# Kernel optimization log

Hardware: AMD Instinct MI355X
Metric: run time of the kernel (lower is better)

Reference implementation:

```python
import jax, jax.numpy as jnp
import numpy as np

N_NODES = 50000
N_EDGES = 512000
D = 128          # node_state_dim
H = 256          # edge hidden / message dim = 2*D (GRU input size)


def _edge_mlp(x, W1, b1, W2, b2):
    # Linear -> ReLU -> Linear, matching nn.Sequential built in build_model
    h = jax.nn.relu(x @ W1.T + b1)
    return h @ W2.T + b2


def _prop_once(node_states, f_idx, t_idx, W1, b1, W2, b2):
    # gather endpoints, concat, edge MLP, scatter-add into destination nodes
    edge_in = jnp.concatenate([node_states[f_idx], node_states[t_idx]], axis=-1)  # [E, 2D]
    msgs = _edge_mlp(edge_in, W1, b1, W2, b2)                                     # [E, H]
    return jax.ops.segment_sum(msgs, t_idx, num_segments=N_NODES)                 # [N, H]


def _gru_cell(x, h, W_ih, W_hh, b_ih, b_hh):
    # PyTorch GRU cell convention
    gi = x @ W_ih.T + b_ih   # [N, 3D]
    gh = h @ W_hh.T + b_hh   # [N, 3D]
    ir, iz, inn = jnp.split(gi, 3, axis=-1)
    hr, hz, hn = jnp.split(gh, 3, axis=-1)
    r = jax.nn.sigmoid(ir + hr)
    z = jax.nn.sigmoid(iz + hz)
    n = jnp.tanh(inn + r * hn)
    return (1.0 - z) * n + z * h


def setup_inputs() -> dict:
    key = jax.random.key(0)
    ks = jax.random.split(key, 16)
    s = 0.1  # edge_net_init_scale-ish small init
    inp = {
        "node_states": jax.random.normal(ks[0], (N_NODES, D), dtype=jnp.float32),
        "from_idx": jax.random.randint(ks[1], (N_EDGES,), 0, N_NODES),
        "to_idx": jax.random.randint(ks[2], (N_EDGES,), 0, N_NODES),
        # forward message net: Linear(2D->H), Linear(H->H)
        "Wf1": jax.random.normal(ks[3], (H, 2 * D), dtype=jnp.float32) * s,
        "bf1": jnp.zeros((H,), jnp.float32),
        "Wf2": jax.random.normal(ks[4], (H, H), dtype=jnp.float32) * s,
        "bf2": jnp.zeros((H,), jnp.float32),
        # reverse message net (separate params)
        "Wr1": jax.random.normal(ks[5], (H, 2 * D), dtype=jnp.float32) * s,
        "br1": jnp.zeros((H,), jnp.float32),
        "Wr2": jax.random.normal(ks[6], (H, H), dtype=jnp.float32) * s,
        "br2": jnp.zeros((H,), jnp.float32),
        # GRU(input=2D, hidden=D) params, torch layout
        "W_ih": jax.random.normal(ks[7], (3 * D, 2 * D), dtype=jnp.float32) * 0.05,
        "W_hh": jax.random.normal(ks[8], (3 * D, D), dtype=jnp.float32) * 0.05,
        "b_ih": jnp.zeros((3 * D,), jnp.float32),
        "b_hh": jnp.zeros((3 * D,), jnp.float32),
    }
    return inp


def reference(node_states, from_idx, to_idx, Wf1, bf1, Wf2, bf2,
              Wr1, br1, Wr2, br2, W_ih, W_hh, b_ih, b_hh):
    agg = _prop_once(node_states, from_idx, to_idx, Wf1, bf1, Wf2, bf2)
    agg = agg + _prop_once(node_states, to_idx, from_idx, Wr1, br1, Wr2, br2)
    return _gru_cell(agg, node_states, W_ih, W_hh, b_ih, b_hh)  # [N, D]
```

## Files before the change

### kernel.cpp

```cpp
#include <hip/hip_runtime.h>
#include <stdint.h>


#define NN 50000
#define NE 512000
#define SCAN_N (2 * NN)
#define SCAN_BLOCKS ((SCAN_N + 1023) / 1024)

typedef unsigned short u16;
typedef unsigned int u32;
using h8  = __attribute__((ext_vector_type(8))) _Float16;
using f4v = __attribute__((ext_vector_type(4))) float;

__device__ __forceinline__ float h2f(u16 u) {
  _Float16 h; __builtin_memcpy(&h, &u, 2); return (float)h;
}
__device__ __forceinline__ u16 f2h(float f) {
  _Float16 h = (_Float16)f; u16 u; __builtin_memcpy(&u, &h, 2); return u;
}
__device__ __forceinline__ float4 load4h(const u16* p) {
  ushort4 u = *(const ushort4*)p;
  return make_float4(h2f(u.x), h2f(u.y), h2f(u.z), h2f(u.w));
}


__global__ void k_wcat(const float* __restrict__ Wf1, const float* __restrict__ bf1,
                       const float* __restrict__ Wr1, const float* __restrict__ br1,
                       u16* __restrict__ Wc16, float* __restrict__ biascat) {
  int c = blockIdx.x;
  int k = threadIdx.x;
  const float* src;
  if (c < 256)      src = Wf1 + (size_t)c * 256;
  else if (c < 512) src = Wr1 + (size_t)(c - 256) * 256 + 128;
  else if (c < 768) src = Wf1 + (size_t)(c - 512) * 256 + 128;
  else              src = Wr1 + (size_t)(c - 768) * 256;
  float v = src[k];
  int nt = c >> 4, kt = k >> 5, g = (k & 31) >> 3, j = k & 7;
  int lane = (c & 15) + g * 16;
  Wc16[((size_t)nt * 4 + kt) * 512 + lane * 8 + j] = f2h(v);
  if (k == 0) biascat[c] = (c < 256) ? bf1[c] : ((c >= 768) ? br1[c - 768] : 0.f);
}

__global__ void k_gcat(const float* __restrict__ W_ih, const float* __restrict__ Wf2,
                       const float* __restrict__ Wr2, u16* __restrict__ G16) {
  int b = blockIdx.x;
  int c = b % 384, w = b / 384;
  const float* W2 = w ? Wr2 : Wf2;
  int k = threadIdx.x;
  float acc = 0.f;
  for (int o = 0; o < 256; ++o)
    acc = fmaf(W_ih[(size_t)c * 256 + o], W2[(size_t)o * 256 + k], acc);
  int kg = w * 256 + k;
  int nt = c >> 4, kt = kg >> 5, g = (kg & 31) >> 3, j = kg & 7;
  int lane = (c & 15) + g * 16;
  G16[((size_t)nt * 16 + kt) * 512 + lane * 8 + j] = f2h(acc);
}

__global__ void k_whh(const float* __restrict__ W_hh, u16* __restrict__ Wh16) {
  int c = blockIdx.x, k = threadIdx.x;
  float v = W_hh[(size_t)c * 128 + k];
  int nt = c >> 4, kt = k >> 5, g = (k & 31) >> 3, j = k & 7;
  int lane = (c & 15) + g * 16;
  Wh16[((size_t)nt * 4 + kt) * 512 + lane * 8 + j] = f2h(v);
}

__global__ void k_vbias(const float* __restrict__ W_ih, const float* __restrict__ bf2,
                        const float* __restrict__ br2, float* __restrict__ vf,
                        float* __restrict__ vr) {
  int c = blockIdx.x * blockDim.x + threadIdx.x;
  if (c >= 384) return;
  float a = 0.f, b = 0.f;
  for (int o = 0; o < 256; ++o) {
    float w = W_ih[(size_t)c * 256 + o];
    a = fmaf(w, bf2[o], a);
    b = fmaf(w, br2[o], b);
  }
  vf[c] = a; vr[c] = b;
}

__global__ void k_nsh(const float* __restrict__ ns, u16* __restrict__ nsf) {
  int t = blockIdx.x * 256 + threadIdx.x;
  int n = t >> 4, kk8 = t & 15;
  float4 v0 = *(const float4*)(ns + (size_t)n * 128 + kk8 * 8);
  float4 v1 = *(const float4*)(ns + (size_t)n * 128 + kk8 * 8 + 4);
  u16 hv[8] = {f2h(v0.x), f2h(v0.y), f2h(v0.z), f2h(v0.w),
               f2h(v1.x), f2h(v1.y), f2h(v1.z), f2h(v1.w)};
  int mt = n >> 4, r = n & 15, kt = kk8 >> 2, g = kk8 & 3;
  int lane = r + g * 16;
  *(uint4*)(nsf + ((size_t)mt * 4 + kt) * 512 + lane * 8) = *(const uint4*)hv;
}

__global__ void k_hist(const int* __restrict__ from, const int* __restrict__ to,
                       int* __restrict__ cnt) {
  int e = blockIdx.x * 256 + threadIdx.x;
  if (e < NE) {
    atomicAdd(cnt + to[e], 1);
    atomicAdd(cnt + NN + from[e], 1);
  }
}

__global__ __launch_bounds__(256) void k_scanA(const int* __restrict__ cnt,
                                               int* __restrict__ bsum) {
  __shared__ int part[256];
  int b = blockIdx.x, tid = threadIdx.x;
  int idx = b * 1024 + tid * 4;
  int s = 0;
  if (idx + 3 < SCAN_N) {
    int4 v = *(const int4*)(cnt + idx);
    s = v.x + v.y + v.z + v.w;
  } else {
    for (int q = 0; q < 4; ++q)
      if (idx + q < SCAN_N) s += cnt[idx + q];
  }
  part[tid] = s;
  __syncthreads();
  for (int d = 128; d > 0; d >>= 1) {
    if (tid < d) part[tid] += part[tid + d];
    __syncthreads();
  }
  if (tid == 0) bsum[b] = part[0];
}

__global__ __launch_bounds__(128) void k_scanB(int* __restrict__ bsum) {
  __shared__ int part[128];
  int tid = threadIdx.x;
  int v = (tid < SCAN_BLOCKS) ? bsum[tid] : 0;
  part[tid] = v;
  __syncthreads();
  for (int d = 1; d < 128; d <<= 1) {
    int x = (tid >= d) ? part[tid - d] : 0;
    __syncthreads();
    part[tid] += x;
    __syncthreads();
  }
  if (tid < SCAN_BLOCKS) bsum[tid] = (tid > 0) ? part[tid - 1] : 0;
}

__global__ __launch_bounds__(256) void k_scanC(const int* __restrict__ cnt,
                                               const int* __restrict__ bsum,
                                               int* __restrict__ off,
                                               int* __restrict__ cur) {
  __shared__ int part[256];
  int b = blockIdx.x, tid = threadIdx.x;
  int idx = b * 1024 + tid * 4;
  int c[4] = {0, 0, 0, 0};
  if (idx + 3 < SCAN_N) {
    int4 v = *(const int4*)(cnt + idx);
    c[0] = v.x; c[1] = v.y; c[2] = v.z; c[3] = v.w;
  } else {
    for (int q = 0; q < 4; ++q)
      if (idx + q < SCAN_N) c[q] = cnt[idx + q];
  }
  int s = c[0] + c[1] + c[2] + c[3];
  part[tid] = s;
  __syncthreads();
  for (int d = 1; d < 256; d <<= 1) {
    int x = (tid >= d) ? part[tid - d] : 0;
    __syncthreads();
    part[tid] += x;
    __syncthreads();
  }
  int run = bsum[b] + ((tid > 0) ? part[tid - 1] : 0);
#pragma unroll
  for (int q = 0; q < 4; ++q) {
    if (idx + q < SCAN_N) {
      off[idx + q] = run;
      cur[idx + q] = run;
      run += c[q];
    }
  }
  if (b == 0 && tid == 0) off[SCAN_N] = 2 * NE;
}

__global__ void k_fill(const int* __restrict__ from, const int* __restrict__ to,
                       int* __restrict__ cur, int* __restrict__ nbr) {
  int e = blockIdx.x * 256 + threadIdx.x;
  if (e < NE) {
    int f = from[e], t = to[e];
    nbr[atomicAdd(cur + t, 1)] = f;
    nbr[atomicAdd(cur + NN + f, 1)] = t;
  }
}

__global__ __launch_bounds__(256) void k_proj(const u16* __restrict__ nsf,
                                              const u16* __restrict__ Wc16,
                                              const float* __restrict__ biascat,
                                              u16* __restrict__ T) {
  const int w = threadIdx.x >> 6, lane = threadIdx.x & 63;
  const int mt0 = blockIdx.x * 4;
  const int nt0 = blockIdx.y * 16 + w * 4;
  const h8 hzv = {(_Float16)0.f, (_Float16)0.f, (_Float16)0.f, (_Float16)0.f,
                  (_Float16)0.f, (_Float16)0.f, (_Float16)0.f, (_Float16)0.f};
  f4v acc[4][4];
#pragma unroll
  for (int m = 0; m < 4; ++m)
#pragma unroll
    for (int n = 0; n < 4; ++n) acc[m][n] = (f4v){0.f, 0.f, 0.f, 0.f};

#pragma unroll
  for (int kt = 0; kt < 4; ++kt) {
    h8 a[4], b[4];
#pragma unroll
    for (int m = 0; m < 4; ++m) {
      int mt = mt0 + m;
      a[m] = (mt < 3125) ? *(const h8*)(nsf + ((size_t)mt * 4 + kt) * 512 + lane * 8) : hzv;
    }
#pragma unroll
    for (int n = 0; n < 4; ++n)
      b[n] = *(const h8*)(Wc16 + ((size_t)(nt0 + n) * 4 + kt) * 512 + lane * 8);
#pragma unroll
    for (int m = 0; m < 4; ++m)
#pragma unroll
      for (int n = 0; n < 4; ++n)
        acc[m][n] = __builtin_amdgcn_mfma_f32_16x16x32_f16(a[m], b[n], acc[m][n], 0, 0, 0);
  }

  const int c0 = lane & 15, rB = (lane >> 4) * 4;
#pragma unroll
  for (int m = 0; m < 4; ++m) {
    int mt = mt0 + m;
    if (mt >= 3125) continue;
#pragma unroll
    for (int n = 0; n < 4; ++n) {
      int col = (nt0 + n) * 16 + c0;
      float bias = biascat[col];
#pragma unroll
      for (int reg = 0; reg < 4; ++reg) {
        int row = mt * 16 + rB + reg;
        T[(size_t)row * 1024 + col] = f2h(acc[m][n][reg] + bias);
      }
    }
  }
}

__global__ __launch_bounds__(256) void k_gather(const u16* __restrict__ T,
                                                const int* __restrict__ nbr,
                                                const int* __restrict__ off,
                                                u16* __restrict__ Sf) {
  const int lane = threadIdx.x & 63;
  const int gid = blockIdx.x * 4 + (threadIdx.x >> 6);
  const int n = gid >> 1, dir = gid & 1;
  const u16* Tn = T + (size_t)n * 1024;
  const int mt = n >> 4, r = n & 15;
  const int g = (lane & 7) >> 1, j0 = (lane & 1) * 4;
  const int laneF = r + g * 16;

  const int invofs = dir ? 256 : 512;
  const int gofs = dir ? 768 : 0;
  float4 inv = load4h(Tn + invofs + lane * 4);
  const int s = off[dir * NN + n];
  const int e = off[dir * NN + n + 1];
  float4 a0 = make_float4(0.f, 0.f, 0.f, 0.f);
  float4 a1 = make_float4(0.f, 0.f, 0.f, 0.f);
  float4 a2 = make_float4(0.f, 0.f, 0.f, 0.f);
  float4 a3 = make_float4(0.f, 0.f, 0.f, 0.f);
  for (int i = s; i < e; i += 64) {
    int nb = (i + lane < e) ? nbr[i + lane] : 0;
    int cnt = min(64, e - i);
    int k = 0;
    for (; k + 3 < cnt; k += 4) {
      int f0 = __shfl(nb, k);
      int f1 = __shfl(nb, k + 1);
      int f2 = __shfl(nb, k + 2);
      int f3 = __shfl(nb, k + 3);
      float4 v0 = load4h(T + (size_t)f0 * 1024 + gofs + lane * 4);
      float4 v1 = load4h(T + (size_t)f1 * 1024 + gofs + lane * 4);
      float4 v2 = load4h(T + (size_t)f2 * 1024 + gofs + lane * 4);
      float4 v3 = load4h(T + (size_t)f3 * 1024 + gofs + lane * 4);
      a0.x += fmaxf(inv.x + v0.x, 0.f); a1.x += fmaxf(inv.x + v1.x, 0.f);
      a0.y += fmaxf(inv.y + v0.y, 0.f); a1.y += fmaxf(inv.y + v1.y, 0.f);
      a0.z += fmaxf(inv.z + v0.z, 0.f); a1.z += fmaxf(inv.z + v1.z, 0.f);
      a0.w += fmaxf(inv.w + v0.w, 0.f); a1.w += fmaxf(inv.w + v1.w, 0.f);
      a2.x += fmaxf(inv.x + v2.x, 0.f); a3.x += fmaxf(inv.x + v3.x, 0.f);
      a2.y += fmaxf(inv.y + v2.y, 0.f); a3.y += fmaxf(inv.y + v3.y, 0.f);
      a2.z += fmaxf(inv.z + v2.z, 0.f); a3.z += fmaxf(inv.z + v3.z, 0.f);
      a2.w += fmaxf(inv.w + v2.w, 0.f); a3.w += fmaxf(inv.w + v3.w, 0.f);
    }
    for (; k < cnt; ++k) {
      int f0 = __shfl(nb, k);
      float4 v0 = load4h(T + (size_t)f0 * 1024 + gofs + lane * 4);
      a0.x += fmaxf(inv.x + v0.x, 0.f);
      a0.y += fmaxf(inv.y + v0.y, 0.f);
      a0.z += fmaxf(inv.z + v0.z, 0.f);
      a0.w += fmaxf(inv.w + v0.w, 0.f);
    }
  }
  a0.x += a1.x + a2.x + a3.x;
  a0.y += a1.y + a2.y + a3.y;
  a0.z += a1.z + a2.z + a3.z;
  a0.w += a1.w + a2.w + a3.w;
  int kt = dir * 8 + (lane >> 3);
  u16 hv[4] = {f2h(a0.x), f2h(a0.y), f2h(a0.z), f2h(a0.w)};
  *(ushort4*)(Sf + ((size_t)mt * 16 + kt) * 512 + laneF * 8 + j0) = *(const ushort4*)hv;
}

__global__ __launch_bounds__(256) void k_gru(const u16* __restrict__ Sf,
                                             const u16* __restrict__ nsf,
                                             const u16* __restrict__ G16,
                                             const u16* __restrict__ Wh16,
                                             const float* __restrict__ ns,
                                             const float* __restrict__ b_ih,
                                             const float* __restrict__ b_hh,
                                             const float* __restrict__ vf,
                                             const float* __restrict__ vr,
                                             const int* __restrict__ off,
                                             float* __restrict__ out) {
  const int w = threadIdx.x >> 6, lane = threadIdx.x & 63;
  const int mt = blockIdx.x >> 1, half = blockIdx.x & 1;
  const int base = half * 4 + w;

  f4v gh[3], gi[3];
#pragma unroll
  for (int g = 0; g < 3; ++g) {
    gh[g] = (f4v){0.f, 0.f, 0.f, 0.f};
    gi[g] = (f4v){0.f, 0.f, 0.f, 0.f};
  }

#pragma unroll
  for (int kt = 0; kt < 4; ++kt) {
    h8 a = *(const h8*)(nsf + ((size_t)mt * 4 + kt) * 512 + lane * 8);
#pragma unroll
    for (int g = 0; g < 3; ++g) {
      h8 b = *(const h8*)(Wh16 + ((size_t)(base + 8 * g) * 4 + kt) * 512 + lane * 8);
      gh[g] = __builtin_amdgcn_mfma_f32_16x16x32_f16(a, b, gh[g], 0, 0, 0);
    }
  }

#pragma unroll
  for (int kt = 0; kt < 16; ++kt) {
    h8 a = *(const h8*)(Sf + ((size_t)mt * 16 + kt) * 512 + lane * 8);
#pragma unroll
    for (int g = 0; g < 3; ++g) {
      h8 b = *(const h8*)(G16 + ((size_t)(base + 8 * g) * 16 + kt) * 512 + lane * 8);
      gi[g] = __builtin_amdgcn_mfma_f32_16x16x32_f16(a, b, gi[g], 0, 0, 0);
    }
  }

  const int c0 = lane & 15, rB = (lane >> 4) * 4;
  const int d = base * 16 + c0;
  const float vf0 = vf[d], vf1 = vf[128 + d], vf2 = vf[256 + d];
  const float vr0 = vr[d], vr1 = vr[128 + d], vr2 = vr[256 + d];
  const float bi0 = b_ih[d], bi1 = b_ih[128 + d], bi2 = b_ih[256 + d];
  const float bh0 = b_hh[d], bh1 = b_hh[128 + d], bh2 = b_hh[256 + d];
#pragma unroll
  for (int reg = 0; reg < 4; ++reg) {
    int row = mt * 16 + rB + reg;
    float idg = (float)(off[row + 1] - off[row]);
    float odg = (float)(off[NN + row + 1] - off[NN + row]);
    float gr = gi[0][reg] + idg * vf0 + odg * vr0 + bi0;
    float gz = gi[1][reg] + idg * vf1 + odg * vr1 + bi1;
    float gn = gi[2][reg] + idg * vf2 + odg * vr2 + bi2;
    float hr = gh[0][reg] + bh0;
    float hzv = gh[1][reg] + bh1;
    float hn = gh[2][reg] + bh2;
    float rg = 1.f / (1.f + __expf(-(gr + hr)));
    float zg = 1.f / (1.f + __expf(-(gz + hzv)));
    float ng = tanhf(gn + rg * hn);
    float h = ns[(size_t)row * 128 + d];
    out[(size_t)row * 128 + d] = (1.f - zg) * ng + zg * h;
  }
}

extern "C" void kernel_launch(void* const* d_in, const int* in_sizes, int n_in,
                              void* d_out, int out_size, void* d_ws, size_t ws_size,
                              hipStream_t stream) {
  const float* ns   = (const float*)d_in[0];
  const int* from   = (const int*)d_in[1];
  const int* to     = (const int*)d_in[2];
  const float* Wf1  = (const float*)d_in[3];
  const float* bf1  = (const float*)d_in[4];
  const float* Wf2  = (const float*)d_in[5];
  const float* bf2  = (const float*)d_in[6];
  const float* Wr1  = (const float*)d_in[7];
  const float* br1  = (const float*)d_in[8];
  const float* Wr2  = (const float*)d_in[9];
  const float* br2  = (const float*)d_in[10];
  const float* W_ih = (const float*)d_in[11];
  const float* W_hh = (const float*)d_in[12];
  const float* b_ih = (const float*)d_in[13];
  const float* b_hh = (const float*)d_in[14];
  float* out = (float*)d_out;

  char* w = (char*)d_ws;
  u16*   Wc16    = (u16*)(w + 0);
  float* biascat = (float*)(w + 262144);
  u16*   G16     = (u16*)(w + 266240);
  u16*   Wh16    = (u16*)(w + 659456);
  float* vf      = (float*)(w + 757760);
  float* vr      = (float*)(w + 759296);
  int*   cnt     = (int*)(w + 760832);
  int*   off     = (int*)(w + 1160960);
  int*   cur     = (int*)(w + 1561088);
  int*   bsum    = (int*)(w + 1961216);
  int*   nbr     = (int*)(w + 1961728);
  u16*   nsf     = (u16*)(w + 6057728);
  u16*   T       = (u16*)(w + 18857728);
  u16*   Sf      = (u16*)(w + 121257728);

  hipMemsetAsync(cnt, 0, 400000, stream);

  k_wcat<<<1024, 128, 0, stream>>>(Wf1, bf1, Wr1, br1, Wc16, biascat);
  k_gcat<<<768, 256, 0, stream>>>(W_ih, Wf2, Wr2, G16);
  k_whh<<<384, 128, 0, stream>>>(W_hh, Wh16);
  k_vbias<<<3, 128, 0, stream>>>(W_ih, bf2, br2, vf, vr);
  k_nsh<<<3125, 256, 0, stream>>>(ns, nsf);

  k_hist<<<(NE + 255) / 256, 256, 0, stream>>>(from, to, cnt);
  k_scanA<<<SCAN_BLOCKS, 256, 0, stream>>>(cnt, bsum);
  k_scanB<<<1, 128, 0, stream>>>(bsum);
  k_scanC<<<SCAN_BLOCKS, 256, 0, stream>>>(cnt, bsum, off, cur);
  k_fill<<<(NE + 255) / 256, 256, 0, stream>>>(from, to, cur, nbr);

  k_proj<<<dim3(782, 4), 256, 0, stream>>>(nsf, Wc16, biascat, T);
  k_gather<<<25000, 256, 0, stream>>>(T, nbr, off, Sf);
  k_gru<<<6250, 256, 0, stream>>>(Sf, nsf, G16, Wh16, ns, b_ih, b_hh, vf, vr, off, out);
}
```

Before: 363.9 us.

## Use packed fp16 add/relu in gather and two row tiles per GRU wave

The gather kernel now keeps neighbor rows in fp16 and applies add+ReLU with packed half2 ops. It also unrolls to 8 outstanding loads per iteration to raise memory-level parallelism. The GRU kernel processes two 16-row tiles per wave, so each weight fragment load feeds two MFMAs, and the grid is halved. This trades more registers per wave and fp16 rounding of the pre-activation sum for fewer weight loads and fewer conversions.

```diff
diff --git a/kernel.cpp b/kernel.cpp
--- a/kernel.cpp
+++ b/kernel.cpp
@@ -9,6 +9,8 @@
 
 typedef unsigned short u16;
 typedef unsigned int u32;
+using h2  = __attribute__((ext_vector_type(2))) _Float16;
+using h4  = __attribute__((ext_vector_type(4))) _Float16;
 using h8  = __attribute__((ext_vector_type(8))) _Float16;
 using f4v = __attribute__((ext_vector_type(4))) float;
 
@@ -17,10 +19,6 @@
 }
 __device__ __forceinline__ u16 f2h(float f) {
   _Float16 h = (_Float16)f; u16 u; __builtin_memcpy(&u, &h, 2); return u;
-}
-__device__ __forceinline__ float4 load4h(const u16* p) {
-  ushort4 u = *(const ushort4*)p;
-  return make_float4(h2f(u.x), h2f(u.y), h2f(u.z), h2f(u.w));
 }
 
 
@@ -247,50 +245,66 @@
 
   const int invofs = dir ? 256 : 512;
   const int gofs = dir ? 768 : 0;
-  float4 inv = load4h(Tn + invofs + lane * 4);
+  const h2 z2 = {(_Float16)0.f, (_Float16)0.f};
+  h4 invv = *(const h4*)(Tn + invofs + lane * 4);
+  h2 inv01 = {invv[0], invv[1]};
+  h2 inv23 = {invv[2], invv[3]};
   const int s = off[dir * NN + n];
   const int e = off[dir * NN + n + 1];
-  float4 a0 = make_float4(0.f, 0.f, 0.f, 0.f);
-  float4 a1 = make_float4(0.f, 0.f, 0.f, 0.f);
-  float4 a2 = make_float4(0.f, 0.f, 0.f, 0.f);
-  float4 a3 = make_float4(0.f, 0.f, 0.f, 0.f);
+  float a0 = 0.f, a1 = 0.f, a2 = 0.f, a3 = 0.f;
+
   for (int i = s; i < e; i += 64) {
     int nb = (i + lane < e) ? nbr[i + lane] : 0;
     int cnt = min(64, e - i);
     int k = 0;
-    for (; k + 3 < cnt; k += 4) {
-      int f0 = __shfl(nb, k);
-      int f1 = __shfl(nb, k + 1);
-      int f2 = __shfl(nb, k + 2);
-      int f3 = __shfl(nb, k + 3);
-      float4 v0 = load4h(T + (size_t)f0 * 1024 + gofs + lane * 4);
-      float4 v1 = load4h(T + (size_t)f1 * 1024 + gofs + lane * 4);
-      float4 v2 = load4h(T + (size_t)f2 * 1024 + gofs + lane * 4);
-      float4 v3 = load4h(T + (size_t)f3 * 1024 + gofs + lane * 4);
-      a0.x += fmaxf(inv.x + v0.x, 0.f); a1.x += fmaxf(inv.x + v1.x, 0.f);
-      a0.y += fmaxf(inv.y + v0.y, 0.f); a1.y += fmaxf(inv.y + v1.y, 0.f);
-      a0.z += fmaxf(inv.z + v0.z, 0.f); a1.z += fmaxf(inv.z + v1.z, 0.f);
-      a0.w += fmaxf(inv.w + v0.w, 0.f); a1.w += fmaxf(inv.w + v1.w, 0.f);
-      a2.x += fmaxf(inv.x + v2.x, 0.f); a3.x += fmaxf(inv.x + v3.x, 0.f);
-      a2.y += fmaxf(inv.y + v2.y, 0.f); a3.y += fmaxf(inv.y + v3.y, 0.f);
-      a2.z += fmaxf(inv.z + v2.z, 0.f); a3.z += fmaxf(inv.z + v3.z, 0.f);
-      a2.w += fmaxf(inv.w + v2.w, 0.f); a3.w += fmaxf(inv.w + v3.w, 0.f);
+    for (; k + 7 < cnt; k += 8) {
+      h4 wv[8];
+#pragma unroll
+      for (int q = 0; q < 8; ++q) {
+        int f = __shfl(nb, k + q);
+        wv[q] = *(const h4*)(T + (size_t)f * 1024 + gofs + lane * 4);
+      }
+#pragma unroll
+      for (int q = 0; q < 8; ++q) {
+        h2 t01 = {wv[q][0], wv[q][1]};
+        h2 t23 = {wv[q][2], wv[q][3]};
+        t01 = __builtin_elementwise_max(t01 + inv01, z2);
+        t23 = __builtin_elementwise_max(t23 + inv23, z2);
+        a0 += (float)t01[0]; a1 += (float)t01[1];
+        a2 += (float)t23[0]; a3 += (float)t23[1];
+      }
+    }
+    if (k + 3 < cnt) {
+      h4 wv[4];
+#pragma unroll
+      for (int q = 0; q < 4; ++q) {
+        int f = __shfl(nb, k + q);
+        wv[q] = *(const h4*)(T + (size_t)f * 1024 + gofs + lane * 4);
+      }
+#pragma unroll
+      for (int q = 0; q < 4; ++q) {
+        h2 t01 = {wv[q][0], wv[q][1]};
+        h2 t23 = {wv[q][2], wv[q][3]};
+        t01 = __builtin_elementwise_max(t01 + inv01, z2);
+        t23 = __builtin_elementwise_max(t23 + inv23, z2);
+        a0 += (float)t01[0]; a1 += (float)t01[1];
+        a2 += (float)t23[0]; a3 += (float)t23[1];
+      }
+      k += 4;
     }
     for (; k < cnt; ++k) {
-      int f0 = __shfl(nb, k);
-      float4 v0 = load4h(T + (size_t)f0 * 1024 + gofs + lane * 4);
-      a0.x += fmaxf(inv.x + v0.x, 0.f);
-      a0.y += fmaxf(inv.y + v0.y, 0.f);
-      a0.z += fmaxf(inv.z + v0.z, 0.f);
-      a0.w += fmaxf(inv.w + v0.w, 0.f);
-    }
-  }
-  a0.x += a1.x + a2.x + a3.x;
-  a0.y += a1.y + a2.y + a3.y;
-  a0.z += a1.z + a2.z + a3.z;
-  a0.w += a1.w + a2.w + a3.w;
+      int f = __shfl(nb, k);
+      h4 wv = *(const h4*)(T + (size_t)f * 1024 + gofs + lane * 4);
+      h2 t01 = {wv[0], wv[1]};
+      h2 t23 = {wv[2], wv[3]};
+      t01 = __builtin_elementwise_max(t01 + inv01, z2);
+      t23 = __builtin_elementwise_max(t23 + inv23, z2);
+      a0 += (float)t01[0]; a1 += (float)t01[1];
+      a2 += (float)t23[0]; a3 += (float)t23[1];
+    }
+  }
   int kt = dir * 8 + (lane >> 3);
-  u16 hv[4] = {f2h(a0.x), f2h(a0.y), f2h(a0.z), f2h(a0.w)};
+  u16 hv[4] = {f2h(a0), f2h(a1), f2h(a2), f2h(a3)};
   *(ushort4*)(Sf + ((size_t)mt * 16 + kt) * 512 + laneF * 8 + j0) = *(const ushort4*)hv;
 }
 
@@ -306,33 +320,42 @@
                                              const int* __restrict__ off,
                                              float* __restrict__ out) {
   const int w = threadIdx.x >> 6, lane = threadIdx.x & 63;
-  const int mt = blockIdx.x >> 1, half = blockIdx.x & 1;
+  const int mt0 = (blockIdx.x >> 1) * 2, half = blockIdx.x & 1;
   const int base = half * 4 + w;
-
-  f4v gh[3], gi[3];
-#pragma unroll
-  for (int g = 0; g < 3; ++g) {
-    gh[g] = (f4v){0.f, 0.f, 0.f, 0.f};
-    gi[g] = (f4v){0.f, 0.f, 0.f, 0.f};
-  }
+  const bool has1 = (mt0 + 1) < 3125;
+  const h8 hz = {(_Float16)0.f, (_Float16)0.f, (_Float16)0.f, (_Float16)0.f,
+                 (_Float16)0.f, (_Float16)0.f, (_Float16)0.f, (_Float16)0.f};
+
+  f4v gh[2][3], gi[2][3];
+#pragma unroll
+  for (int m = 0; m < 2; ++m)
+#pragma unroll
+    for (int g = 0; g < 3; ++g) {
+      gh[m][g] = (f4v){0.f, 0.f, 0.f, 0.f};
+      gi[m][g] = (f4v){0.f, 0.f, 0.f, 0.f};
+    }
 
 #pragma unroll
   for (int kt = 0; kt < 4; ++kt) {
-    h8 a = *(const h8*)(nsf + ((size_t)mt * 4 + kt) * 512 + lane * 8);
+    h8 a0 = *(const h8*)(nsf + ((size_t)mt0 * 4 + kt) * 512 + lane * 8);
+    h8 a1 = has1 ? *(const h8*)(nsf + ((size_t)(mt0 + 1) * 4 + kt) * 512 + lane * 8) : hz;
 #pragma unroll
     for (int g = 0; g < 3; ++g) {
       h8 b = *(const h8*)(Wh16 + ((size_t)(base + 8 * g) * 4 + kt) * 512 + lane * 8);
-      gh[g] = __builtin_amdgcn_mfma_f32_16x16x32_f16(a, b, gh[g], 0, 0, 0);
+      gh[0][g] = __builtin_amdgcn_mfma_f32_16x16x32_f16(a0, b, gh[0][g], 0, 0, 0);
+      gh[1][g] = __builtin_amdgcn_mfma_f32_16x16x32_f16(a1, b, gh[1][g], 0, 0, 0);
     }
   }
 
 #pragma unroll
   for (int kt = 0; kt < 16; ++kt) {
-    h8 a = *(const h8*)(Sf + ((size_t)mt * 16 + kt) * 512 + lane * 8);
+    h8 a0 = *(const h8*)(Sf + ((size_t)mt0 * 16 + kt) * 512 + lane * 8);
+    h8 a1 = has1 ? *(const h8*)(Sf + ((size_t)(mt0 + 1) * 16 + kt) * 512 + lane * 8) : hz;
 #pragma unroll
     for (int g = 0; g < 3; ++g) {
       h8 b = *(const h8*)(G16 + ((size_t)(base + 8 * g) * 16 + kt) * 512 + lane * 8);
-      gi[g] = __builtin_amdgcn_mfma_f32_16x16x32_f16(a, b, gi[g], 0, 0, 0);
+      gi[0][g] = __builtin_amdgcn_mfma_f32_16x16x32_f16(a0, b, gi[0][g], 0, 0, 0);
+      gi[1][g] = __builtin_amdgcn_mfma_f32_16x16x32_f16(a1, b, gi[1][g], 0, 0, 0);
     }
   }
 
@@ -343,21 +366,26 @@
   const float bi0 = b_ih[d], bi1 = b_ih[128 + d], bi2 = b_ih[256 + d];
   const float bh0 = b_hh[d], bh1 = b_hh[128 + d], bh2 = b_hh[256 + d];
 #pragma unroll
-  for (int reg = 0; reg < 4; ++reg) {
-    int row = mt * 16 + rB + reg;
-    float idg = (float)(off[row + 1] - off[row]);
-    float odg = (float)(off[NN + row + 1] - off[NN + row]);
-    float gr = gi[0][reg] + idg * vf0 + odg * vr0 + bi0;
-    float gz = gi[1][reg] + idg * vf1 + odg * vr1 + bi1;
-    float gn = gi[2][reg] + idg * vf2 + odg * vr2 + bi2;
-    float hr = gh[0][reg] + bh0;
-    float hzv = gh[1][reg] + bh1;
-    float hn = gh[2][reg] + bh2;
-    float rg = 1.f / (1.f + __expf(-(gr + hr)));
-    float zg = 1.f / (1.f + __expf(-(gz + hzv)));
-    float ng = tanhf(gn + rg * hn);
-    float h = ns[(size_t)row * 128 + d];
-    out[(size_t)row * 128 + d] = (1.f - zg) * ng + zg * h;
+  for (int m = 0; m < 2; ++m) {
+    if (m == 1 && !has1) continue;
+    const int mt = mt0 + m;
+#pragma unroll
+    for (int reg = 0; reg < 4; ++reg) {
+      int row = mt * 16 + rB + reg;
+      float idg = (float)(off[row + 1] - off[row]);
+      float odg = (float)(off[NN + row + 1] - off[NN + row]);
+      float gr = gi[m][0][reg] + idg * vf0 + odg * vr0 + bi0;
+      float gz = gi[m][1][reg] + idg * vf1 + odg * vr1 + bi1;
+      float gn = gi[m][2][reg] + idg * vf2 + odg * vr2 + bi2;
+      float hr = gh[m][0][reg] + bh0;
+      float hzv = gh[m][1][reg] + bh1;
+      float hn = gh[m][2][reg] + bh2;
+      float rg = 1.f / (1.f + __expf(-(gr + hr)));
+      float zg = 1.f / (1.f + __expf(-(gz + hzv)));
+      float ng = tanhf(gn + rg * hn);
+      float h = ns[(size_t)row * 128 + d];
+      out[(size_t)row * 128 + d] = (1.f - zg) * ng + zg * h;
+    }
   }
 }
 
@@ -413,5 +441,5 @@
 
   k_proj<<<dim3(782, 4), 256, 0, stream>>>(nsf, Wc16, biascat, T);
   k_gather<<<25000, 256, 0, stream>>>(T, nbr, off, Sf);
-  k_gru<<<6250, 256, 0, stream>>>(Sf, nsf, G16, Wh16, ns, b_ih, b_hh, vf, vr, off, out);
-}
+  k_gru<<<3126, 256, 0, stream>>>(Sf, nsf, G16, Wh16, ns, b_ih, b_hh, vf, vr, off, out);
+}
```

Measured after the change: 348.6 us. 4.2% less time.
